# Kernel optimization log

Hardware: AMD Instinct MI355X
Metric: run time of the kernel (lower is better)

## Reference

```python
import jax, jax.numpy as jnp
import numpy as np


def _gcn_conv(x, edge_index, W, b):
    # PyG GCNConv: h = D^{-1/2} (A + I) D^{-1/2} (x @ W) + b
    n = x.shape[0]
    xw = x @ W  # [N, C]
    loop = jnp.arange(n, dtype=edge_index.dtype)
    row = jnp.concatenate([edge_index[0], loop])  # source (x_j)
    col = jnp.concatenate([edge_index[1], loop])  # target (aggregation index)
    deg = jax.ops.segment_sum(jnp.ones_like(col, dtype=xw.dtype), col, num_segments=n)
    dinv = jnp.where(deg > 0, deg ** -0.5, 0.0)
    norm = dinv[row] * dinv[col]  # [E+N]
    out = jax.ops.segment_sum(xw[row] * norm[:, None], col, num_segments=n)
    return out + b


def setup_inputs() -> dict:
    key = jax.random.key(0)
    ks = jax.random.split(key, 8)
    N, F, E = 100000, 512, 3200000
    W_SCALE = 0.1  # keep sigmoid un-saturated
    x = jax.random.normal(ks[0], (N, F), dtype=jnp.float32)
    edge_index = jax.random.randint(ks[1], (2, E), 0, N, dtype=jnp.int64)
    Wg = jax.random.normal(ks[2], (F, 16), dtype=jnp.float32) * W_SCALE
    bg = jnp.zeros((16,), dtype=jnp.float32)
    W1 = jax.random.normal(ks[3], (16, 16), dtype=jnp.float32) * W_SCALE
    b1 = jnp.zeros((16,), dtype=jnp.float32)
    W2 = jax.random.normal(ks[4], (16, 32), dtype=jnp.float32) * W_SCALE
    b2 = jnp.zeros((32,), dtype=jnp.float32)
    W3 = jax.random.normal(ks[5], (32, 1), dtype=jnp.float32) * W_SCALE
    b3 = jnp.zeros((1,), dtype=jnp.float32)
    return {"x": x, "edge_index": edge_index, "Wg": Wg, "bg": bg,
            "W1": W1, "b1": b1, "W2": W2, "b2": b2, "W3": W3, "b3": b3}


def reference(x, edge_index, Wg, bg, W1, b1, W2, b2, W3, b3):
    h = jax.nn.relu(_gcn_conv(x, edge_index, Wg, bg))
    h = jax.nn.relu(h @ W1 + b1)
    h = jax.nn.relu(h @ W2 + b2)
    return jax.nn.sigmoid(h @ W3 + b3)  # [N, 1]
```

## Files before the change

### kernel.cpp

```cpp
#include <hip/hip_runtime.h>
#include <math.h>


static constexpr int F = 512;
static constexpr int C = 16;
static constexpr int BSH = 7;
static constexpr int BSZ = 128;
static constexpr int NBMAX = 1024;
static constexpr int EPB = 16384;

__global__ __launch_bounds__(256) void k_xw(const float* __restrict__ x,
                                            const float* __restrict__ Wg,
                                            float* __restrict__ xw, int n)
{
    int row = blockIdx.x * 256 + threadIdx.x;
    if (row >= n) return;
    float acc[C];
#pragma unroll
    for (int c = 0; c < C; ++c) acc[c] = 0.f;
    const float4* xr = (const float4*)(x + (size_t)row * F);
#pragma unroll 4
    for (int k4 = 0; k4 < F / 4; ++k4) {
        float4 xv = xr[k4];
        const float* w = Wg + k4 * 4 * C;
#pragma unroll
        for (int j = 0; j < 4; ++j) {
            float xs = (j == 0) ? xv.x : (j == 1) ? xv.y : (j == 2) ? xv.z : xv.w;
#pragma unroll
            for (int c = 0; c < C; ++c)
                acc[c] = fmaf(xs, w[j * C + c], acc[c]);
        }
    }
    float4* o = (float4*)(xw + (size_t)row * C);
#pragma unroll
    for (int q = 0; q < 4; ++q)
        o[q] = make_float4(acc[4 * q + 0], acc[4 * q + 1], acc[4 * q + 2], acc[4 * q + 3]);
}

__global__ __launch_bounds__(256) void k_bcount(const int* __restrict__ dst,
                                                int* __restrict__ bh, int E)
{
    __shared__ int hist[NBMAX];
    for (int i = threadIdx.x; i < NBMAX; i += 256) hist[i] = 0;
    __syncthreads();
    int base = blockIdx.x * EPB;
#pragma unroll 4
    for (int j = 0; j < EPB / 256; ++j) {
        int e = base + j * 256 + threadIdx.x;
        if (e < E) atomicAdd(&hist[dst[e] >> BSH], 1);
    }
    __syncthreads();
    int* row = bh + (size_t)blockIdx.x * NBMAX;
    for (int i = threadIdx.x; i < NBMAX; i += 256) row[i] = hist[i];
}

__global__ __launch_bounds__(256) void k_colscan(int* __restrict__ bh,
                                                 int* __restrict__ total, int geb)
{
    int b = blockIdx.x * 256 + threadIdx.x;
    int run = 0;
#pragma unroll 4
    for (int g = 0; g < geb; ++g) {
        size_t idx = (size_t)g * NBMAX + b;
        int v = bh[idx];
        bh[idx] = run;
        run += v;
    }
    total[b] = run;
}

__global__ __launch_bounds__(1024) void k_bscan(const int* __restrict__ total,
                                                int* __restrict__ bstart)
{
    __shared__ int sh[NBMAX];
    int t = threadIdx.x;
    int v = total[t];
    sh[t] = v;
    __syncthreads();
    for (int d = 1; d < NBMAX; d <<= 1) {
        int u = (t >= d) ? sh[t - d] : 0;
        __syncthreads();
        sh[t] += u;
        __syncthreads();
    }
    bstart[t] = sh[t] - v;
    if (t == NBMAX - 1) bstart[NBMAX] = sh[t];
}

__global__ __launch_bounds__(256) void k_bscatter(const int* __restrict__ ei,
                                                  const int* __restrict__ bh,
                                                  const int* __restrict__ bstart,
                                                  int* __restrict__ packed, int E)
{
    __shared__ int cur[NBMAX];
    int g = blockIdx.x;
    const int* row = bh + (size_t)g * NBMAX;
    for (int i = threadIdx.x; i < NBMAX; i += 256) cur[i] = bstart[i] + row[i];
    __syncthreads();
    int base = g * EPB;
#pragma unroll 2
    for (int j = 0; j < EPB / 256; ++j) {
        int e = base + j * 256 + threadIdx.x;
        if (e < E) {
            int d = ei[E + e];
            int s = ei[e];
            int b = d >> BSH;
            int r = atomicAdd(&cur[b], 1);
            packed[r] = s | ((d & (BSZ - 1)) << 17);
        }
    }
}

__global__ __launch_bounds__(256) void k_bcsr(const int* __restrict__ packed,
                                              const int* __restrict__ bstart,
                                              float* __restrict__ y,
                                              int* __restrict__ srcs,
                                              int* __restrict__ starts,
                                              int* __restrict__ cnt,
                                              float* __restrict__ dinv, int n)
{
    int b = blockIdx.x, t = threadIdx.x;
    __shared__ int hist[BSZ];
    __shared__ int sc[BSZ];
    __shared__ float sdi[BSZ];
    if (t < BSZ) hist[t] = 0;
    __syncthreads();
    int beg = bstart[b], end = bstart[b + 1];
    for (int e = beg + t; e < end; e += 256)
        atomicAdd(&hist[(packed[e] >> 17) & (BSZ - 1)], 1);
    __syncthreads();
    int myc = 0;
    if (t < BSZ) { myc = hist[t]; sc[t] = myc; }
    __syncthreads();
    for (int d = 1; d < BSZ; d <<= 1) {
        int u = 0;
        if (t < BSZ && t >= d) u = sc[t - d];
        __syncthreads();
        if (t < BSZ) sc[t] += u;
        __syncthreads();
    }
    int node0 = b << BSH;
    if (t < BSZ) {
        int lst = sc[t] - myc;
        sc[t] = lst;
        float di = rsqrtf((float)(myc + 1));
        sdi[t] = di;
        int node = node0 + t;
        if (node < n) { starts[node] = beg + lst; cnt[node] = myc; dinv[node] = di; }
        hist[t] = 0;
    }
    __syncthreads();
    for (int e = beg + t; e < end; e += 256) {
        int p = packed[e];
        int dl = (p >> 17) & (BSZ - 1);
        int r = atomicAdd(&hist[dl], 1);
        srcs[beg + sc[dl] + r] = p & 0x1FFFF;
    }
    int nn = n - node0; if (nn > BSZ) nn = BSZ;
    if (nn <= 0) return;
    int lim = nn * 4;
    float4* yv = (float4*)(y + (size_t)node0 * C);
    for (int i = t; i < lim; i += 256) {
        float di = sdi[i >> 2];
        float4 v = yv[i];
        v.x *= di; v.y *= di; v.z *= di; v.w *= di;
        yv[i] = v;
    }
}

__global__ __launch_bounds__(256) void k_gather_mlp(const float* __restrict__ y,
                                                    const int* __restrict__ srcs,
                                                    const int* __restrict__ starts,
                                                    const int* __restrict__ cnt,
                                                    const float* __restrict__ dinv,
                                                    const float* __restrict__ bg,
                                                    const float* __restrict__ W1,
                                                    const float* __restrict__ b1,
                                                    const float* __restrict__ W2,
                                                    const float* __restrict__ b2,
                                                    const float* __restrict__ W3,
                                                    const float* __restrict__ b3,
                                                    float* __restrict__ out, int n)
{
    __shared__ float sh[64][17];
    int tid = threadIdx.x;
    int gtid = blockIdx.x * 256 + tid;
    int i = gtid >> 2;
    int q = tid & 3;
    if (i < n) {
        const float4* yv = (const float4*)y;
        float4 acc = yv[(size_t)i * 4 + q];
        int beg = starts[i];
        int end = beg + cnt[i];
        int e = beg;
        int headEnd = (beg + 3) & ~3;
        if (headEnd > end) headEnd = end;
        for (; e < headEnd; ++e) {
            float4 v = yv[(size_t)srcs[e] * 4 + q];
            acc.x += v.x; acc.y += v.y; acc.z += v.z; acc.w += v.w;
        }
        for (; e + 4 <= end; e += 4) {
            int4 s4 = *(const int4*)(srcs + e);
            float4 v0 = yv[(size_t)s4.x * 4 + q];
            float4 v1 = yv[(size_t)s4.y * 4 + q];
            float4 v2 = yv[(size_t)s4.z * 4 + q];
            float4 v3 = yv[(size_t)s4.w * 4 + q];
            acc.x += v0.x + v1.x + v2.x + v3.x;
            acc.y += v0.y + v1.y + v2.y + v3.y;
            acc.z += v0.z + v1.z + v2.z + v3.z;
            acc.w += v0.w + v1.w + v2.w + v3.w;
        }
        for (; e < end; ++e) {
            float4 v = yv[(size_t)srcs[e] * 4 + q];
            acc.x += v.x; acc.y += v.y; acc.z += v.z; acc.w += v.w;
        }
        float di = dinv[i];
        const float* bq = bg + q * 4;
        int lr = tid >> 2;
        sh[lr][4 * q + 0] = fmaxf(fmaf(acc.x, di, bq[0]), 0.f);
        sh[lr][4 * q + 1] = fmaxf(fmaf(acc.y, di, bq[1]), 0.f);
        sh[lr][4 * q + 2] = fmaxf(fmaf(acc.z, di, bq[2]), 0.f);
        sh[lr][4 * q + 3] = fmaxf(fmaf(acc.w, di, bq[3]), 0.f);
    }
    __syncthreads();
    if (tid < 64) {
        int node = blockIdx.x * 64 + tid;
        if (node < n) {
            float h[16];
#pragma unroll
            for (int k = 0; k < 16; ++k) h[k] = sh[tid][k];
            float h1[16];
#pragma unroll
            for (int c = 0; c < 16; ++c) {
                float s = b1[c];
#pragma unroll
                for (int k = 0; k < 16; ++k) s = fmaf(h[k], W1[k * 16 + c], s);
                h1[c] = fmaxf(s, 0.f);
            }
            float h2[32];
#pragma unroll
            for (int c = 0; c < 32; ++c) {
                float s = b2[c];
#pragma unroll
                for (int k = 0; k < 16; ++k) s = fmaf(h1[k], W2[k * 32 + c], s);
                h2[c] = fmaxf(s, 0.f);
            }
            float s = b3[0];
#pragma unroll
            for (int k = 0; k < 32; ++k) s = fmaf(h2[k], W3[k], s);
            out[node] = 1.f / (1.f + expf(-s));
        }
    }
}

extern "C" void kernel_launch(void* const* d_in, const int* in_sizes, int n_in,
                              void* d_out, int out_size, void* d_ws, size_t ws_size,
                              hipStream_t stream)
{
    const float* x  = (const float*)d_in[0];
    const int*   ei = (const int*)d_in[1];
    const float* Wg = (const float*)d_in[2];
    const float* bg = (const float*)d_in[3];
    const float* W1 = (const float*)d_in[4];
    const float* b1 = (const float*)d_in[5];
    const float* W2 = (const float*)d_in[6];
    const float* b2 = (const float*)d_in[7];
    const float* W3 = (const float*)d_in[8];
    const float* b3 = (const float*)d_in[9];
    float* out = (float*)d_out;

    int n = in_sizes[0] / F;
    int E = in_sizes[1] / 2;

    int gb  = (n + 255) / 256;
    int geb = (E + EPB - 1) / EPB;
    int NB  = (n + BSZ - 1) >> BSH;

    char* ws = (char*)d_ws;
    size_t off = 0;
    float* y      = (float*)(ws + off); off += (size_t)n * C * sizeof(float);
    off += (size_t)n * C * sizeof(float);
    int*   packed = (int*)  (ws + off); off += (size_t)E * sizeof(int);
    int*   srcs   = (int*)  (ws + off);
    int*   bh     = srcs;
    size_t big = (size_t)E; if ((size_t)geb * NBMAX > big) big = (size_t)geb * NBMAX;
    off += big * sizeof(int);
    int*   starts = (int*)  (ws + off); off += (size_t)((n + 3) & ~3) * sizeof(int);
    int*   cnt    = (int*)  (ws + off); off += (size_t)((n + 3) & ~3) * sizeof(int);
    float* dinv   = (float*)(ws + off); off += (size_t)((n + 3) & ~3) * sizeof(float);
    int*   total  = (int*)  (ws + off); off += NBMAX * sizeof(int);
    int*   bstart = (int*)  (ws + off);

    k_xw<<<gb, 256, 0, stream>>>(x, Wg, y, n);
    k_bcount<<<geb, 256, 0, stream>>>(ei + E, bh, E);
    k_colscan<<<NBMAX / 256, 256, 0, stream>>>(bh, total, geb);
    k_bscan<<<1, 1024, 0, stream>>>(total, bstart);
    k_bscatter<<<geb, 256, 0, stream>>>(ei, bh, bstart, packed, E);
    k_bcsr<<<NB, 256, 0, stream>>>(packed, bstart, y, srcs, starts, cnt, dinv, n);
    k_gather_mlp<<<(n + 63) / 64, 256, 0, stream>>>(y, srcs, starts, cnt, dinv, bg,
                                                    W1, b1, W2, b2, W3, b3, out, n);
}
```

Before: 503.8 us.

## Fuse xw matmul with bucket histogram and merge column/bucket scans

Launches the x@W projection and the destination-bucket histogram as one grid, with the extra blocks doing the counting, so the two independent passes overlap and one launch is saved. Merges the per-bucket column scan and the bucket prefix scan into a single 1024-thread kernel that batches 16 loads per step. This removes two kernel launches and the intermediate total buffer. The trade-off is that the scan now runs on one workgroup instead of four, and the fused kernel carries shared memory that the matmul blocks never use.

```diff
diff --git a/kernel.cpp b/kernel.cpp
--- a/kernel.cpp
+++ b/kernel.cpp
@@ -9,10 +9,28 @@
 static constexpr int NBMAX = 1024;
 static constexpr int EPB = 16384;
 
-__global__ __launch_bounds__(256) void k_xw(const float* __restrict__ x,
-                                            const float* __restrict__ Wg,
-                                            float* __restrict__ xw, int n)
-{
+__global__ __launch_bounds__(256) void k_xw_bcount(const float* __restrict__ x,
+                                                   const float* __restrict__ Wg,
+                                                   float* __restrict__ xw, int n,
+                                                   const int* __restrict__ dst,
+                                                   int* __restrict__ bh, int E, int gb)
+{
+    if ((int)blockIdx.x >= gb) {
+        __shared__ int hist[NBMAX];
+        for (int i = threadIdx.x; i < NBMAX; i += 256) hist[i] = 0;
+        __syncthreads();
+        int g = blockIdx.x - gb;
+        int base = g * EPB;
+#pragma unroll 4
+        for (int j = 0; j < EPB / 256; ++j) {
+            int e = base + j * 256 + threadIdx.x;
+            if (e < E) atomicAdd(&hist[dst[e] >> BSH], 1);
+        }
+        __syncthreads();
+        int* row = bh + (size_t)g * NBMAX;
+        for (int i = threadIdx.x; i < NBMAX; i += 256) row[i] = hist[i];
+        return;
+    }
     int row = blockIdx.x * 256 + threadIdx.x;
     if (row >= n) return;
     float acc[C];
@@ -37,54 +55,40 @@
         o[q] = make_float4(acc[4 * q + 0], acc[4 * q + 1], acc[4 * q + 2], acc[4 * q + 3]);
 }
 
-__global__ __launch_bounds__(256) void k_bcount(const int* __restrict__ dst,
-                                                int* __restrict__ bh, int E)
-{
-    __shared__ int hist[NBMAX];
-    for (int i = threadIdx.x; i < NBMAX; i += 256) hist[i] = 0;
-    __syncthreads();
-    int base = blockIdx.x * EPB;
-#pragma unroll 4
-    for (int j = 0; j < EPB / 256; ++j) {
-        int e = base + j * 256 + threadIdx.x;
-        if (e < E) atomicAdd(&hist[dst[e] >> BSH], 1);
-    }
-    __syncthreads();
-    int* row = bh + (size_t)blockIdx.x * NBMAX;
-    for (int i = threadIdx.x; i < NBMAX; i += 256) row[i] = hist[i];
-}
-
-__global__ __launch_bounds__(256) void k_colscan(int* __restrict__ bh,
-                                                 int* __restrict__ total, int geb)
-{
-    int b = blockIdx.x * 256 + threadIdx.x;
+__global__ __launch_bounds__(1024) void k_scan(int* __restrict__ bh,
+                                               int* __restrict__ bstart, int geb)
+{
+    int b = threadIdx.x;
     int run = 0;
-#pragma unroll 4
-    for (int g = 0; g < geb; ++g) {
+    int g = 0;
+    for (; g + 16 <= geb; g += 16) {
+        int v[16];
+#pragma unroll
+        for (int j = 0; j < 16; ++j) v[j] = bh[(size_t)(g + j) * NBMAX + b];
+#pragma unroll
+        for (int j = 0; j < 16; ++j) {
+            bh[(size_t)(g + j) * NBMAX + b] = run;
+            run += v[j];
+        }
+    }
+    for (; g < geb; ++g) {
         size_t idx = (size_t)g * NBMAX + b;
         int v = bh[idx];
         bh[idx] = run;
         run += v;
     }
-    total[b] = run;
-}
-
-__global__ __launch_bounds__(1024) void k_bscan(const int* __restrict__ total,
-                                                int* __restrict__ bstart)
-{
     __shared__ int sh[NBMAX];
-    int t = threadIdx.x;
-    int v = total[t];
-    sh[t] = v;
+    int v0 = run;
+    sh[b] = run;
     __syncthreads();
     for (int d = 1; d < NBMAX; d <<= 1) {
-        int u = (t >= d) ? sh[t - d] : 0;
-        __syncthreads();
-        sh[t] += u;
-        __syncthreads();
-    }
-    bstart[t] = sh[t] - v;
-    if (t == NBMAX - 1) bstart[NBMAX] = sh[t];
+        int u = (b >= d) ? sh[b - d] : 0;
+        __syncthreads();
+        sh[b] += u;
+        __syncthreads();
+    }
+    bstart[b] = sh[b] - v0;
+    if (b == NBMAX - 1) bstart[NBMAX] = sh[b];
 }
 
 __global__ __launch_bounds__(256) void k_bscatter(const int* __restrict__ ei,
@@ -279,7 +283,6 @@
     char* ws = (char*)d_ws;
     size_t off = 0;
     float* y      = (float*)(ws + off); off += (size_t)n * C * sizeof(float);
-    off += (size_t)n * C * sizeof(float);
     int*   packed = (int*)  (ws + off); off += (size_t)E * sizeof(int);
     int*   srcs   = (int*)  (ws + off);
     int*   bh     = srcs;
@@ -288,13 +291,10 @@
     int*   starts = (int*)  (ws + off); off += (size_t)((n + 3) & ~3) * sizeof(int);
     int*   cnt    = (int*)  (ws + off); off += (size_t)((n + 3) & ~3) * sizeof(int);
     float* dinv   = (float*)(ws + off); off += (size_t)((n + 3) & ~3) * sizeof(float);
-    int*   total  = (int*)  (ws + off); off += NBMAX * sizeof(int);
     int*   bstart = (int*)  (ws + off);
 
-    k_xw<<<gb, 256, 0, stream>>>(x, Wg, y, n);
-    k_bcount<<<geb, 256, 0, stream>>>(ei + E, bh, E);
-    k_colscan<<<NBMAX / 256, 256, 0, stream>>>(bh, total, geb);
-    k_bscan<<<1, 1024, 0, stream>>>(total, bstart);
+    k_xw_bcount<<<gb + geb, 256, 0, stream>>>(x, Wg, y, n, ei + E, bh, E, gb);
+    k_scan<<<1, 1024, 0, stream>>>(bh, bstart, geb);
     k_bscatter<<<geb, 256, 0, stream>>>(ei, bh, bstart, packed, E);
     k_bcsr<<<NB, 256, 0, stream>>>(packed, bstart, y, srcs, starts, cnt, dinv, n);
     k_gather_mlp<<<(n + 63) / 64, 256, 0, stream>>>(y, srcs, starts, cnt, dinv, bg,
```

New measurement: 484.0 us. 3.9% less time.
